# Kernel tuning notes

Hardware: AMD Instinct MI355X
Metric: run time of the kernel (lower is better)

Reference implementation:

```python
import jax, jax.numpy as jnp
import numpy as np
from jax import lax

B, C, H, W = 32, 64, 112, 112
ALPHA, BETA1, BETA2 = 0.25, 1.0, 1.0

# STE sign for weights (DifferntiableSign): fwd = +/-1, bwd mask |w|<=1 (w in [-1,1))
@jax.custom_vjp
def dsign(w):
    return jnp.where(w >= 0, 1.0, -1.0).astype(w.dtype)
def _dsign_fwd(w):
    return dsign(w), w
def _dsign_bwd(w, g):
    return (g * ((w < 1) & (w >= -1)).astype(g.dtype),)
dsign.defvjp(_dsign_fwd, _dsign_bwd)

# ReActNet BinaryActivation: fwd = sign(x), bwd piecewise-polynomial STE
@jax.custom_vjp
def bin_act(x):
    return jnp.where(x >= 0, 1.0, -1.0).astype(x.dtype)
def _ba_fwd(x):
    return bin_act(x), x
def _ba_bwd(x, g):
    slope = jnp.where((x >= -1) & (x < 0), 2.0 + 2.0 * x,
             jnp.where((x >= 0) & (x < 1), 2.0 - 2.0 * x, 0.0))
    return (g * slope.astype(g.dtype),)
bin_act.defvjp(_ba_fwd, _ba_bwd)

def scaled_sign_conv(x, w):
    # per-output-channel scale = mean(|w|) over (in, kh, kw)
    scale = jnp.mean(jnp.abs(w), axis=(1, 2, 3), keepdims=True)
    wb = scale * dsign(w)
    return lax.conv_general_dilated(x, wb, window_strides=(1, 1),
                                    padding=((1, 1), (1, 1)),
                                    dimension_numbers=("NCHW", "OIHW", "NCHW"))

def add_bias(x, b):
    return x + b[None, :, None, None]

def prelu(x, a):
    return jnp.where(x >= 0, x, a[None, :, None, None] * x)

def setup_inputs() -> dict:
    key = jax.random.key(0)
    ks = jax.random.split(key, 12)
    x = jax.random.normal(ks[0], (B, C, H, W), dtype=jnp.float32)
    # conv weights: symmetric uniform in [-1e-3, 1e-3] so signs are nontrivial
    w3 = (jax.random.uniform(ks[1], (C, C, 3, 3)) - 0.5) * 0.002
    w_pw = (jax.random.uniform(ks[2], (C, C, 3, 3)) - 0.5) * 0.002
    b11 = jax.random.normal(ks[3], (C,)) * 0.01
    b12 = jax.random.normal(ks[4], (C,)) * 0.01
    b13 = jax.random.normal(ks[5], (C,)) * 0.01
    b21 = jax.random.normal(ks[6], (C,)) * 0.01
    b22 = jax.random.normal(ks[7], (C,)) * 0.01
    b23 = jax.random.normal(ks[8], (C,)) * 0.01
    a1 = jax.random.uniform(ks[9], (C,), minval=0.1, maxval=0.4)
    a2 = jax.random.uniform(ks[10], (C,), minval=0.1, maxval=0.4)
    return {"x": x, "w3": w3, "w_pw": w_pw, "b11": b11, "b12": b12, "b13": b13,
            "b21": b21, "b22": b22, "b23": b23, "a1": a1, "a2": a2}

def reference(x, w3, w_pw, b11, b12, b13, b21, b22, b23, a1, a2):
    x_in = x * BETA1
    out1 = add_bias(x_in, b11)            # move11
    out1 = bin_act(out1)
    out1 = scaled_sign_conv(out1, w3)     # binary_3x3
    out1 = x + out1 * ALPHA               # stride==1: residual is original x
    out1 = add_bias(out1, b12)            # move12
    out1 = prelu(out1, a1)
    out1 = add_bias(out1, b13)            # move13
    out1_in = out1 * BETA2
    out2 = add_bias(out1_in, b21)         # move21
    out2 = bin_act(out2)
    out2 = scaled_sign_conv(out2, w_pw)   # binary_pw (3x3 per given defaults)
    out2 = out2 * ALPHA + out1
    out2 = add_bias(out2, b22)            # move22
    out2 = prelu(out2, a2)
    out2 = add_bias(out2, b23)            # move23
    return out2
```

## Files before the change

### kernel.cpp

```cpp
#include <hip/hip_runtime.h>
#include <hip/hip_fp16.h>
#include <stdint.h>

#define Bn 32
#define Cc 64
#define Hh 112
#define Ww 112
#define HWp (Hh*Ww)
#define NPIX (Bn*HWp)
#define PW 114
#define PHW (PW*PW)
#define ALPHA 0.25f

#define WB1_OFF   0
#define WB2_OFF   4608
#define ASC1_OFF  9216
#define ASC2_OFF  9472
#define CI1_OFF   9728
#define CI2_OFF   12032
#define BITS1_OFF 16384
#define BITS2_OFF (16384 + 3326976)
#define OUT1H_OFF (16384 + 2*3326976)
#define WS_NEED   (OUT1H_OFF + (size_t)NPIX*Cc*2)

__global__ __launch_bounds__(64) void prep_weights(
        const float* __restrict__ w3, const float* __restrict__ wpw,
        uint64_t* __restrict__ wb1, uint64_t* __restrict__ wb2,
        float* __restrict__ asc1, float* __restrict__ asc2,
        int* __restrict__ ci1, int* __restrict__ ci2) {
    int b = blockIdx.x;
    int lane = threadIdx.x;
    const float* w  = (b < 64) ? w3   : wpw;
    uint64_t* wbits = (b < 64) ? wb1  : wb2;
    float*    ascp  = (b < 64) ? asc1 : asc2;
    int*      cip   = (b < 64) ? ci1  : ci2;
    int o = b & 63;
    const float* wp = w + ((size_t)o * Cc + lane) * 9;
    float v[9]; float asum = 0.f;
    #pragma unroll
    for (int t = 0; t < 9; ++t) { v[t] = wp[t]; asum += fabsf(v[t]); }
    uint64_t bal[9];
    #pragma unroll
    for (int t = 0; t < 9; ++t) bal[t] = __ballot(v[t] < 0.f);
    if (lane < 9) {
        wbits[o * 9 + lane] = bal[lane];
        int ty = lane, tr = ty / 3, tc = ty % 3;
        int sum = 0;
        #pragma unroll
        for (int t = 0; t < 9; ++t) {
            int r = t / 3, c = t % 3;
            bool inv = (tr == 0 && r == 0) || (tr == 2 && r == 2) ||
                       (tc == 0 && c == 0) || (tc == 2 && c == 2);
            if (inv) sum += 64 - 2 * (int)__popcll(bal[t]);
        }
        cip[o * 9 + ty] = 576 - sum;
    }
    #pragma unroll
    for (int off = 32; off > 0; off >>= 1) asum += __shfl_down(asum, off, 64);
    if (lane == 0) ascp[o] = ALPHA * asum * (1.f / 576.f);
}

__global__ __launch_bounds__(256) void pack1(const float* __restrict__ x,
                                             const float* __restrict__ b11,
                                             uint64_t* __restrict__ bits1,
                                             uint64_t* __restrict__ bits2) {
    int pc = blockIdx.x * 256 + threadIdx.x;
    if (pc >= PHW) return;
    int n = blockIdx.y;
    int ph = pc / PW, pw = pc - ph * PW;
    size_t bi = (size_t)n * PHW + pc;
    if (ph == 0 || ph == PW - 1 || pw == 0 || pw == PW - 1) {
        bits1[bi] = 0; bits2[bi] = 0;
        return;
    }
    int hw = (ph - 1) * Ww + (pw - 1);
    const float* xp = x + (size_t)n * Cc * HWp + hw;
    uint64_t m = 0;
    #pragma unroll 1
    for (int cc = 0; cc < Cc; cc += 16) {
        float v[16];
        #pragma unroll
        for (int j = 0; j < 16; ++j) v[j] = xp[(size_t)(cc + j) * HWp];
        #pragma unroll
        for (int j = 0; j < 16; ++j)
            if (v[j] + b11[cc + j] < 0.f) m |= (1ull << (cc + j));
    }
    bits1[bi] = m;
}

template <typename OutT>
__global__ __launch_bounds__(256, 4) void conv1_ep(
        const float* __restrict__ x, const uint64_t* __restrict__ bits1,
        const uint64_t* __restrict__ wb, const float* __restrict__ asc,
        const int* __restrict__ cint,
        const float* __restrict__ b12, const float* __restrict__ a1,
        const float* __restrict__ b13, const float* __restrict__ b21,
        OutT* __restrict__ out1, uint64_t* __restrict__ bits2) {
    __shared__ int lci[Cc * 12];
    for (int i = threadIdx.x; i < Cc * 9; i += 256) {
        int o = i / 9, ty = i - o * 9;
        lci[o * 12 + ty] = cint[i];
    }
    __syncthreads();

    int hw = blockIdx.x * 256 + threadIdx.x;
    int n = blockIdx.y;
    int h = hw / Ww, w = hw - h * Ww;
    int t9 = ((h == 0) ? 0 : (h == Hh - 1) ? 6 : 3) +
             ((w == 0) ? 0 : (w == Ww - 1) ? 2 : 1);

    const uint64_t* bp = bits1 + (size_t)n * PHW + (h + 1) * PW + (w + 1);
    uint64_t w00 = bp[-PW - 1], w01 = bp[-PW], w02 = bp[-PW + 1];
    uint64_t w10 = bp[-1],      w11 = bp[0],   w12 = bp[1];
    uint64_t w20 = bp[PW - 1],  w21 = bp[PW],  w22 = bp[PW + 1];

    const float* xp = x + (size_t)n * Cc * HWp + hw;
    OutT* op = out1 + (size_t)n * Cc * HWp + hw;
    uint64_t m2 = 0;

    float xv[8], xn[8];
    #pragma unroll
    for (int j = 0; j < 8; ++j) xv[j] = xp[(size_t)j * HWp];

    #pragma unroll 1
    for (int oc = 0; oc < Cc; oc += 8) {
        #pragma unroll
        for (int j = 0; j < 8; ++j) xn[j] = xp[(size_t)((oc + 8 + j) & 63) * HWp];
        #pragma unroll
        for (int j = 0; j < 8; ++j) {
            int o = oc + j;
            const uint64_t* wo = wb + o * 9;
            int s;
            s  = (int)__popcll(w00 ^ wo[0]);
            s += (int)__popcll(w01 ^ wo[1]);
            s += (int)__popcll(w02 ^ wo[2]);
            s += (int)__popcll(w10 ^ wo[3]);
            s += (int)__popcll(w11 ^ wo[4]);
            s += (int)__popcll(w12 ^ wo[5]);
            s += (int)__popcll(w20 ^ wo[6]);
            s += (int)__popcll(w21 ^ wo[7]);
            s += (int)__popcll(w22 ^ wo[8]);
            int m = lci[o * 12 + t9] - (s << 1);
            float v = fmaf(asc[o], (float)m, xv[j]);
            v += b12[o];
            v = v >= 0.f ? v : a1[o] * v;
            v += b13[o];
            op[(size_t)o * HWp] = (OutT)v;
            if (v + b21[o] < 0.f) m2 |= (1ull << o);
        }
        #pragma unroll
        for (int j = 0; j < 8; ++j) xv[j] = xn[j];
    }
    bits2[(size_t)n * PHW + (h + 1) * PW + (w + 1)] = m2;
}

template <typename InT>
__global__ __launch_bounds__(256, 4) void conv2_ep(
        const uint64_t* __restrict__ bits2, const InT* __restrict__ out1,
        const uint64_t* __restrict__ wb, const float* __restrict__ asc,
        const int* __restrict__ cint,
        const float* __restrict__ b22, const float* __restrict__ a2,
        const float* __restrict__ b23, float* __restrict__ out) {
    __shared__ int lci[Cc * 12];
    for (int i = threadIdx.x; i < Cc * 9; i += 256) {
        int o = i / 9, ty = i - o * 9;
        lci[o * 12 + ty] = cint[i];
    }
    __syncthreads();

    int hw = blockIdx.x * 256 + threadIdx.x;
    int n = blockIdx.y;
    int h = hw / Ww, w = hw - h * Ww;
    int t9 = ((h == 0) ? 0 : (h == Hh - 1) ? 6 : 3) +
             ((w == 0) ? 0 : (w == Ww - 1) ? 2 : 1);

    const uint64_t* bp = bits2 + (size_t)n * PHW + (h + 1) * PW + (w + 1);
    uint64_t w00 = bp[-PW - 1], w01 = bp[-PW], w02 = bp[-PW + 1];
    uint64_t w10 = bp[-1],      w11 = bp[0],   w12 = bp[1];
    uint64_t w20 = bp[PW - 1],  w21 = bp[PW],  w22 = bp[PW + 1];

    const InT* ip = out1 + (size_t)n * Cc * HWp + hw;
    float* op = out + (size_t)n * Cc * HWp + hw;

    InT rv[8], rn[8];
    #pragma unroll
    for (int j = 0; j < 8; ++j) rv[j] = ip[(size_t)j * HWp];

    #pragma unroll 1
    for (int oc = 0; oc < Cc; oc += 8) {
        #pragma unroll
        for (int j = 0; j < 8; ++j) rn[j] = ip[(size_t)((oc + 8 + j) & 63) * HWp];
        #pragma unroll
        for (int j = 0; j < 8; ++j) {
            int o = oc + j;
            const uint64_t* wo = wb + o * 9;
            int s;
            s  = (int)__popcll(w00 ^ wo[0]);
            s += (int)__popcll(w01 ^ wo[1]);
            s += (int)__popcll(w02 ^ wo[2]);
            s += (int)__popcll(w10 ^ wo[3]);
            s += (int)__popcll(w11 ^ wo[4]);
            s += (int)__popcll(w12 ^ wo[5]);
            s += (int)__popcll(w20 ^ wo[6]);
            s += (int)__popcll(w21 ^ wo[7]);
            s += (int)__popcll(w22 ^ wo[8]);
            int m = lci[o * 12 + t9] - (s << 1);
            float v = fmaf(asc[o], (float)m, (float)rv[j]);
            v += b22[o];
            v = v >= 0.f ? v : a2[o] * v;
            v += b23[o];
            op[(size_t)o * HWp] = v;
        }
        #pragma unroll
        for (int j = 0; j < 8; ++j) rv[j] = rn[j];
    }
}

extern "C" void kernel_launch(void* const* d_in, const int* in_sizes, int n_in,
                              void* d_out, int out_size, void* d_ws, size_t ws_size,
                              hipStream_t stream) {
    const float* x    = (const float*)d_in[0];
    const float* w3   = (const float*)d_in[1];
    const float* wpw  = (const float*)d_in[2];
    const float* b11  = (const float*)d_in[3];
    const float* b12  = (const float*)d_in[4];
    const float* b13  = (const float*)d_in[5];
    const float* b21  = (const float*)d_in[6];
    const float* b22  = (const float*)d_in[7];
    const float* b23  = (const float*)d_in[8];
    const float* a1   = (const float*)d_in[9];
    const float* a2   = (const float*)d_in[10];

    char* ws = (char*)d_ws;
    uint64_t* wb1   = (uint64_t*)(ws + WB1_OFF);
    uint64_t* wb2   = (uint64_t*)(ws + WB2_OFF);
    float*    asc1  = (float*)(ws + ASC1_OFF);
    float*    asc2  = (float*)(ws + ASC2_OFF);
    int*      ci1   = (int*)(ws + CI1_OFF);
    int*      ci2   = (int*)(ws + CI2_OFF);
    uint64_t* bits1 = (uint64_t*)(ws + BITS1_OFF);
    uint64_t* bits2 = (uint64_t*)(ws + BITS2_OFF);
    float*    out   = (float*)d_out;

    dim3 pgrid((PHW + 255) / 256, Bn);
    dim3 cgrid(HWp / 256, Bn);

    prep_weights<<<128, 64, 0, stream>>>(w3, wpw, wb1, wb2, asc1, asc2, ci1, ci2);
    pack1<<<pgrid, 256, 0, stream>>>(x, b11, bits1, bits2);

    if (ws_size >= WS_NEED) {
        __half* out1h = (__half*)(ws + OUT1H_OFF);
        conv1_ep<__half><<<cgrid, 256, 0, stream>>>(x, bits1, wb1, asc1, ci1,
                                                    b12, a1, b13, b21, out1h, bits2);
        conv2_ep<__half><<<cgrid, 256, 0, stream>>>(bits2, out1h, wb2, asc2, ci2,
                                                    b22, a2, b23, out);
    } else {
        conv1_ep<float><<<cgrid, 256, 0, stream>>>(x, bits1, wb1, asc1, ci1,
                                                   b12, a1, b13, b21, out, bits2);
        conv2_ep<float><<<cgrid, 256, 0, stream>>>(bits2, out, wb2, asc2, ci2,
                                                   b22, a2, b23, out);
    }
}
```

Measured before the change: 293.3 us.

## Preload all 64 channel inputs up front and fully unroll the conv loops

In pack1 and both conv kernels, the code now loads all 64 per-channel inputs into registers at once, pinned with empty asm so the compiler cannot sink the loads. It replaces the 8-wide software-pipelined loop with a fully unrolled 64-channel loop. The shared-memory correction table is transposed so each thread reads a contiguous row chosen by its border type. The aim is more memory-level parallelism from issuing all loads before compute, at the cost of higher register pressure that may reduce occupancy or cause spills under launch_bounds(256,4).

```diff
diff --git a/kernel.cpp b/kernel.cpp
--- a/kernel.cpp
+++ b/kernel.cpp
@@ -22,6 +22,8 @@
 #define BITS2_OFF (16384 + 3326976)
 #define OUT1H_OFF (16384 + 2*3326976)
 #define WS_NEED   (OUT1H_OFF + (size_t)NPIX*Cc*2)
+
+#define PIN(v) asm volatile("" : "+v"(v))
 
 __global__ __launch_bounds__(64) void prep_weights(
         const float* __restrict__ w3, const float* __restrict__ wpw,
@@ -60,10 +62,10 @@
     if (lane == 0) ascp[o] = ALPHA * asum * (1.f / 576.f);
 }
 
-__global__ __launch_bounds__(256) void pack1(const float* __restrict__ x,
-                                             const float* __restrict__ b11,
-                                             uint64_t* __restrict__ bits1,
-                                             uint64_t* __restrict__ bits2) {
+__global__ __launch_bounds__(256, 4) void pack1(const float* __restrict__ x,
+                                                const float* __restrict__ b11,
+                                                uint64_t* __restrict__ bits1,
+                                                uint64_t* __restrict__ bits2) {
     int pc = blockIdx.x * 256 + threadIdx.x;
     if (pc >= PHW) return;
     int n = blockIdx.y;
@@ -75,16 +77,15 @@
     }
     int hw = (ph - 1) * Ww + (pw - 1);
     const float* xp = x + (size_t)n * Cc * HWp + hw;
+    float v[Cc];
+    #pragma unroll
+    for (int j = 0; j < Cc; ++j) v[j] = xp[(size_t)j * HWp];
+    #pragma unroll
+    for (int j = 0; j < Cc; ++j) PIN(v[j]);
     uint64_t m = 0;
-    #pragma unroll 1
-    for (int cc = 0; cc < Cc; cc += 16) {
-        float v[16];
-        #pragma unroll
-        for (int j = 0; j < 16; ++j) v[j] = xp[(size_t)(cc + j) * HWp];
-        #pragma unroll
-        for (int j = 0; j < 16; ++j)
-            if (v[j] + b11[cc + j] < 0.f) m |= (1ull << (cc + j));
-    }
+    #pragma unroll
+    for (int j = 0; j < Cc; ++j)
+        if (v[j] + b11[j] < 0.f) m |= (1ull << j);
     bits1[bi] = m;
 }
 
@@ -96,10 +97,10 @@
         const float* __restrict__ b12, const float* __restrict__ a1,
         const float* __restrict__ b13, const float* __restrict__ b21,
         OutT* __restrict__ out1, uint64_t* __restrict__ bits2) {
-    __shared__ int lci[Cc * 12];
+    __shared__ int lci[10 * Cc];
     for (int i = threadIdx.x; i < Cc * 9; i += 256) {
         int o = i / 9, ty = i - o * 9;
-        lci[o * 12 + ty] = cint[i];
+        lci[ty * Cc + o] = cint[i];
     }
     __syncthreads();
 
@@ -108,6 +109,7 @@
     int h = hw / Ww, w = hw - h * Ww;
     int t9 = ((h == 0) ? 0 : (h == Hh - 1) ? 6 : 3) +
              ((w == 0) ? 0 : (w == Ww - 1) ? 2 : 1);
+    const int* lcit = lci + t9 * Cc;
 
     const uint64_t* bp = bits1 + (size_t)n * PHW + (h + 1) * PW + (w + 1);
     uint64_t w00 = bp[-PW - 1], w01 = bp[-PW], w02 = bp[-PW + 1];
@@ -116,40 +118,34 @@
 
     const float* xp = x + (size_t)n * Cc * HWp + hw;
     OutT* op = out1 + (size_t)n * Cc * HWp + hw;
+
+    float xv[Cc];
+    #pragma unroll
+    for (int j = 0; j < Cc; ++j) xv[j] = xp[(size_t)j * HWp];
+    #pragma unroll
+    for (int j = 0; j < Cc; ++j) PIN(xv[j]);
+
     uint64_t m2 = 0;
-
-    float xv[8], xn[8];
-    #pragma unroll
-    for (int j = 0; j < 8; ++j) xv[j] = xp[(size_t)j * HWp];
-
-    #pragma unroll 1
-    for (int oc = 0; oc < Cc; oc += 8) {
-        #pragma unroll
-        for (int j = 0; j < 8; ++j) xn[j] = xp[(size_t)((oc + 8 + j) & 63) * HWp];
-        #pragma unroll
-        for (int j = 0; j < 8; ++j) {
-            int o = oc + j;
-            const uint64_t* wo = wb + o * 9;
-            int s;
-            s  = (int)__popcll(w00 ^ wo[0]);
-            s += (int)__popcll(w01 ^ wo[1]);
-            s += (int)__popcll(w02 ^ wo[2]);
-            s += (int)__popcll(w10 ^ wo[3]);
-            s += (int)__popcll(w11 ^ wo[4]);
-            s += (int)__popcll(w12 ^ wo[5]);
-            s += (int)__popcll(w20 ^ wo[6]);
-            s += (int)__popcll(w21 ^ wo[7]);
-            s += (int)__popcll(w22 ^ wo[8]);
-            int m = lci[o * 12 + t9] - (s << 1);
-            float v = fmaf(asc[o], (float)m, xv[j]);
-            v += b12[o];
-            v = v >= 0.f ? v : a1[o] * v;
-            v += b13[o];
-            op[(size_t)o * HWp] = (OutT)v;
-            if (v + b21[o] < 0.f) m2 |= (1ull << o);
-        }
-        #pragma unroll
-        for (int j = 0; j < 8; ++j) xv[j] = xn[j];
+    #pragma unroll
+    for (int o = 0; o < Cc; ++o) {
+        const uint64_t* wo = wb + o * 9;
+        int s;
+        s  = (int)__popcll(w00 ^ wo[0]);
+        s += (int)__popcll(w01 ^ wo[1]);
+        s += (int)__popcll(w02 ^ wo[2]);
+        s += (int)__popcll(w10 ^ wo[3]);
+        s += (int)__popcll(w11 ^ wo[4]);
+        s += (int)__popcll(w12 ^ wo[5]);
+        s += (int)__popcll(w20 ^ wo[6]);
+        s += (int)__popcll(w21 ^ wo[7]);
+        s += (int)__popcll(w22 ^ wo[8]);
+        int m = lcit[o] - (s << 1);
+        float v = fmaf(asc[o], (float)m, xv[o]);
+        v += b12[o];
+        v = v >= 0.f ? v : a1[o] * v;
+        v += b13[o];
+        op[(size_t)o * HWp] = (OutT)v;
+        if (v + b21[o] < 0.f) m2 |= (1ull << o);
     }
     bits2[(size_t)n * PHW + (h + 1) * PW + (w + 1)] = m2;
 }
@@ -161,10 +157,10 @@
         const int* __restrict__ cint,
         const float* __restrict__ b22, const float* __restrict__ a2,
         const float* __restrict__ b23, float* __restrict__ out) {
-    __shared__ int lci[Cc * 12];
+    __shared__ int lci[10 * Cc];
     for (int i = threadIdx.x; i < Cc * 9; i += 256) {
         int o = i / 9, ty = i - o * 9;
-        lci[o * 12 + ty] = cint[i];
+        lci[ty * Cc + o] = cint[i];
     }
     __syncthreads();
 
@@ -173,6 +169,7 @@
     int h = hw / Ww, w = hw - h * Ww;
     int t9 = ((h == 0) ? 0 : (h == Hh - 1) ? 6 : 3) +
              ((w == 0) ? 0 : (w == Ww - 1) ? 2 : 1);
+    const int* lcit = lci + t9 * Cc;
 
     const uint64_t* bp = bits2 + (size_t)n * PHW + (h + 1) * PW + (w + 1);
     uint64_t w00 = bp[-PW - 1], w01 = bp[-PW], w02 = bp[-PW + 1];
@@ -182,37 +179,31 @@
     const InT* ip = out1 + (size_t)n * Cc * HWp + hw;
     float* op = out + (size_t)n * Cc * HWp + hw;
 
-    InT rv[8], rn[8];
-    #pragma unroll
-    for (int j = 0; j < 8; ++j) rv[j] = ip[(size_t)j * HWp];
-
-    #pragma unroll 1
-    for (int oc = 0; oc < Cc; oc += 8) {
-        #pragma unroll
-        for (int j = 0; j < 8; ++j) rn[j] = ip[(size_t)((oc + 8 + j) & 63) * HWp];
-        #pragma unroll
-        for (int j = 0; j < 8; ++j) {
-            int o = oc + j;
-            const uint64_t* wo = wb + o * 9;
-            int s;
-            s  = (int)__popcll(w00 ^ wo[0]);
-            s += (int)__popcll(w01 ^ wo[1]);
-            s += (int)__popcll(w02 ^ wo[2]);
-            s += (int)__popcll(w10 ^ wo[3]);
-            s += (int)__popcll(w11 ^ wo[4]);
-            s += (int)__popcll(w12 ^ wo[5]);
-            s += (int)__popcll(w20 ^ wo[6]);
-            s += (int)__popcll(w21 ^ wo[7]);
-            s += (int)__popcll(w22 ^ wo[8]);
-            int m = lci[o * 12 + t9] - (s << 1);
-            float v = fmaf(asc[o], (float)m, (float)rv[j]);
-            v += b22[o];
-            v = v >= 0.f ? v : a2[o] * v;
-            v += b23[o];
-            op[(size_t)o * HWp] = v;
-        }
-        #pragma unroll
-        for (int j = 0; j < 8; ++j) rv[j] = rn[j];
+    float rv[Cc];
+    #pragma unroll
+    for (int j = 0; j < Cc; ++j) rv[j] = (float)ip[(size_t)j * HWp];
+    #pragma unroll
+    for (int j = 0; j < Cc; ++j) PIN(rv[j]);
+
+    #pragma unroll
+    for (int o = 0; o < Cc; ++o) {
+        const uint64_t* wo = wb + o * 9;
+        int s;
+        s  = (int)__popcll(w00 ^ wo[0]);
+        s += (int)__popcll(w01 ^ wo[1]);
+        s += (int)__popcll(w02 ^ wo[2]);
+        s += (int)__popcll(w10 ^ wo[3]);
+        s += (int)__popcll(w11 ^ wo[4]);
+        s += (int)__popcll(w12 ^ wo[5]);
+        s += (int)__popcll(w20 ^ wo[6]);
+        s += (int)__popcll(w21 ^ wo[7]);
+        s += (int)__popcll(w22 ^ wo[8]);
+        int m = lcit[o] - (s << 1);
+        float v = fmaf(asc[o], (float)m, rv[o]);
+        v += b22[o];
+        v = v >= 0.f ? v : a2[o] * v;
+        v += b23[o];
+        op[(size_t)o * HWp] = v;
     }
 }
 
```

Result: slower. 312.7 us (+6.6%).

## Process two horizontal pixels per thread with vectorized loads and shared weight reuse

Applied to the files above, without the earlier changes.

Each thread in pack1, conv1 and conv2 now handles two adjacent pixels, using float2/half2 vector loads and stores. The 3x3 bit-neighbourhood becomes a 3x4 window, so bit loads overlap between the two outputs and each weight word is loaded once for both pixels. pack1 now zeroes only the border cells in separate blocks. The final output is written with nontemporal stores, and the correction-count table is repacked to stride 10 with a moved offset. In exchange, per-thread register pressure rises and the grid has half as many threads, which may reduce occupancy.

```diff
diff --git a/kernel.cpp b/kernel.cpp
--- a/kernel.cpp
+++ b/kernel.cpp
@@ -10,18 +10,25 @@
 #define NPIX (Bn*HWp)
 #define PW 114
 #define PHW (PW*PW)
+#define NPAIR (HWp/2)
+#define WROW (Ww/2)
 #define ALPHA 0.25f
+
+typedef float    f32x2 __attribute__((ext_vector_type(2)));
+typedef _Float16 f16x2 __attribute__((ext_vector_type(2)));
 
 #define WB1_OFF   0
 #define WB2_OFF   4608
 #define ASC1_OFF  9216
 #define ASC2_OFF  9472
 #define CI1_OFF   9728
-#define CI2_OFF   12032
+#define CI2_OFF   12288
 #define BITS1_OFF 16384
 #define BITS2_OFF (16384 + 3326976)
 #define OUT1H_OFF (16384 + 2*3326976)
 #define WS_NEED   (OUT1H_OFF + (size_t)NPIX*Cc*2)
+
+#define MEMFENCE() asm volatile("" ::: "memory")
 
 __global__ __launch_bounds__(64) void prep_weights(
         const float* __restrict__ w3, const float* __restrict__ wpw,
@@ -53,39 +60,66 @@
                        (tc == 0 && c == 0) || (tc == 2 && c == 2);
             if (inv) sum += 64 - 2 * (int)__popcll(bal[t]);
         }
-        cip[o * 9 + ty] = 576 - sum;
+        cip[o * 10 + ty] = 576 - sum;
     }
     #pragma unroll
     for (int off = 32; off > 0; off >>= 1) asum += __shfl_down(asum, off, 64);
     if (lane == 0) ascp[o] = ALPHA * asum * (1.f / 576.f);
 }
 
-__global__ __launch_bounds__(256) void pack1(const float* __restrict__ x,
-                                             const float* __restrict__ b11,
-                                             uint64_t* __restrict__ bits1,
-                                             uint64_t* __restrict__ bits2) {
-    int pc = blockIdx.x * 256 + threadIdx.x;
-    if (pc >= PHW) return;
+__global__ __launch_bounds__(256, 4) void pack1(const float* __restrict__ x,
+                                                const float* __restrict__ b11,
+                                                uint64_t* __restrict__ bits1,
+                                                uint64_t* __restrict__ bits2) {
     int n = blockIdx.y;
-    int ph = pc / PW, pw = pc - ph * PW;
-    size_t bi = (size_t)n * PHW + pc;
-    if (ph == 0 || ph == PW - 1 || pw == 0 || pw == PW - 1) {
-        bits1[bi] = 0; bits2[bi] = 0;
+    if (blockIdx.x >= 25) {
+        int t = (blockIdx.x - 25) * 256 + threadIdx.x;
+        if (t < 2 * PW + 2 * Hh) {
+            int cell;
+            if      (t < PW)          cell = t;
+            else if (t < 2 * PW)      cell = 113 * PW + (t - PW);
+            else if (t < 2 * PW + Hh) cell = (t - 2 * PW + 1) * PW;
+            else                      cell = (t - 2 * PW - Hh + 1) * PW + 113;
+            size_t bi = (size_t)n * PHW + cell;
+            bits1[bi] = 0; bits2[bi] = 0;
+        }
         return;
     }
-    int hw = (ph - 1) * Ww + (pw - 1);
+    int p = blockIdx.x * 256 + threadIdx.x;
+    if (p >= NPAIR) return;
+    int h = p / WROW, w0 = (p - h * WROW) * 2;
+    int hw = h * Ww + w0;
     const float* xp = x + (size_t)n * Cc * HWp + hw;
-    uint64_t m = 0;
+    size_t bi = (size_t)n * PHW + (h + 1) * PW + (w0 + 1);
+
+    f32x2 cur[16], nxt[16];
+    #pragma unroll
+    for (int j = 0; j < 16; ++j) cur[j] = *(const f32x2*)(xp + (size_t)j * HWp);
+
+    uint64_t ma = 0, mb = 0;
     #pragma unroll 1
-    for (int cc = 0; cc < Cc; cc += 16) {
-        float v[16];
-        #pragma unroll
-        for (int j = 0; j < 16; ++j) v[j] = xp[(size_t)(cc + j) * HWp];
+    for (int cc = 0; cc < Cc - 16; cc += 16) {
         #pragma unroll
         for (int j = 0; j < 16; ++j)
-            if (v[j] + b11[cc + j] < 0.f) m |= (1ull << (cc + j));
-    }
-    bits1[bi] = m;
+            nxt[j] = *(const f32x2*)(xp + (size_t)(cc + 16 + j) * HWp);
+        MEMFENCE();
+        #pragma unroll
+        for (int j = 0; j < 16; ++j) {
+            float bb = b11[cc + j];
+            if (cur[j].x + bb < 0.f) ma |= (1ull << (cc + j));
+            if (cur[j].y + bb < 0.f) mb |= (1ull << (cc + j));
+        }
+        MEMFENCE();
+        #pragma unroll
+        for (int j = 0; j < 16; ++j) cur[j] = nxt[j];
+    }
+    #pragma unroll
+    for (int j = 0; j < 16; ++j) {
+        float bb = b11[48 + j];
+        if (cur[j].x + bb < 0.f) ma |= (1ull << (48 + j));
+        if (cur[j].y + bb < 0.f) mb |= (1ull << (48 + j));
+    }
+    bits1[bi] = ma; bits1[bi + 1] = mb;
 }
 
 template <typename OutT>
@@ -96,62 +130,77 @@
         const float* __restrict__ b12, const float* __restrict__ a1,
         const float* __restrict__ b13, const float* __restrict__ b21,
         OutT* __restrict__ out1, uint64_t* __restrict__ bits2) {
-    __shared__ int lci[Cc * 12];
-    for (int i = threadIdx.x; i < Cc * 9; i += 256) {
-        int o = i / 9, ty = i - o * 9;
-        lci[o * 12 + ty] = cint[i];
-    }
+    __shared__ int lci[Cc * 10];
+    for (int i = threadIdx.x; i < Cc * 10; i += 256) lci[i] = cint[i];
     __syncthreads();
 
-    int hw = blockIdx.x * 256 + threadIdx.x;
+    int p = blockIdx.x * 256 + threadIdx.x;
+    if (p >= NPAIR) return;
     int n = blockIdx.y;
-    int h = hw / Ww, w = hw - h * Ww;
-    int t9 = ((h == 0) ? 0 : (h == Hh - 1) ? 6 : 3) +
-             ((w == 0) ? 0 : (w == Ww - 1) ? 2 : 1);
-
-    const uint64_t* bp = bits1 + (size_t)n * PHW + (h + 1) * PW + (w + 1);
-    uint64_t w00 = bp[-PW - 1], w01 = bp[-PW], w02 = bp[-PW + 1];
-    uint64_t w10 = bp[-1],      w11 = bp[0],   w12 = bp[1];
-    uint64_t w20 = bp[PW - 1],  w21 = bp[PW],  w22 = bp[PW + 1];
+    int h = p / WROW, w0 = (p - h * WROW) * 2;
+    int hw = h * Ww + w0;
+    int rowp = (h == 0) ? 0 : (h == Hh - 1) ? 6 : 3;
+    int t9a = rowp + ((w0 == 0) ? 0 : 1);
+    int t9b = rowp + ((w0 + 1 == Ww - 1) ? 2 : 1);
+
+    const uint64_t* bp = bits1 + (size_t)n * PHW + (h + 1) * PW + (w0 + 1);
+    uint64_t q0[4], q1[4], q2[4];
+    #pragma unroll
+    for (int c = 0; c < 4; ++c) {
+        q0[c] = bp[-PW - 1 + c]; q1[c] = bp[-1 + c]; q2[c] = bp[PW - 1 + c];
+    }
 
     const float* xp = x + (size_t)n * Cc * HWp + hw;
     OutT* op = out1 + (size_t)n * Cc * HWp + hw;
-    uint64_t m2 = 0;
-
-    float xv[8], xn[8];
-    #pragma unroll
-    for (int j = 0; j < 8; ++j) xv[j] = xp[(size_t)j * HWp];
+    uint64_t m2a = 0, m2b = 0;
+
+    f32x2 cur[8], nxt[8];
+    #pragma unroll
+    for (int j = 0; j < 8; ++j) cur[j] = *(const f32x2*)(xp + (size_t)j * HWp);
 
     #pragma unroll 1
-    for (int oc = 0; oc < Cc; oc += 8) {
-        #pragma unroll
-        for (int j = 0; j < 8; ++j) xn[j] = xp[(size_t)((oc + 8 + j) & 63) * HWp];
+    for (int oc = 0; oc <= Cc - 8; oc += 8) {
+        if (oc < Cc - 8) {
+            #pragma unroll
+            for (int j = 0; j < 8; ++j)
+                nxt[j] = *(const f32x2*)(xp + (size_t)(oc + 8 + j) * HWp);
+        }
+        MEMFENCE();
         #pragma unroll
         for (int j = 0; j < 8; ++j) {
             int o = oc + j;
             const uint64_t* wo = wb + o * 9;
-            int s;
-            s  = (int)__popcll(w00 ^ wo[0]);
-            s += (int)__popcll(w01 ^ wo[1]);
-            s += (int)__popcll(w02 ^ wo[2]);
-            s += (int)__popcll(w10 ^ wo[3]);
-            s += (int)__popcll(w11 ^ wo[4]);
-            s += (int)__popcll(w12 ^ wo[5]);
-            s += (int)__popcll(w20 ^ wo[6]);
-            s += (int)__popcll(w21 ^ wo[7]);
-            s += (int)__popcll(w22 ^ wo[8]);
-            int m = lci[o * 12 + t9] - (s << 1);
-            float v = fmaf(asc[o], (float)m, xv[j]);
-            v += b12[o];
-            v = v >= 0.f ? v : a1[o] * v;
-            v += b13[o];
-            op[(size_t)o * HWp] = (OutT)v;
-            if (v + b21[o] < 0.f) m2 |= (1ull << o);
-        }
-        #pragma unroll
-        for (int j = 0; j < 8; ++j) xv[j] = xn[j];
-    }
-    bits2[(size_t)n * PHW + (h + 1) * PW + (w + 1)] = m2;
+            uint64_t t0 = wo[0], t1 = wo[1], t2 = wo[2], t3 = wo[3], t4 = wo[4],
+                     t5 = wo[5], t6 = wo[6], t7 = wo[7], t8 = wo[8];
+            int sa = (int)__popcll(q0[0] ^ t0) + (int)__popcll(q0[1] ^ t1) + (int)__popcll(q0[2] ^ t2)
+                   + (int)__popcll(q1[0] ^ t3) + (int)__popcll(q1[1] ^ t4) + (int)__popcll(q1[2] ^ t5)
+                   + (int)__popcll(q2[0] ^ t6) + (int)__popcll(q2[1] ^ t7) + (int)__popcll(q2[2] ^ t8);
+            int sb = (int)__popcll(q0[1] ^ t0) + (int)__popcll(q0[2] ^ t1) + (int)__popcll(q0[3] ^ t2)
+                   + (int)__popcll(q1[1] ^ t3) + (int)__popcll(q1[2] ^ t4) + (int)__popcll(q1[3] ^ t5)
+                   + (int)__popcll(q2[1] ^ t6) + (int)__popcll(q2[2] ^ t7) + (int)__popcll(q2[3] ^ t8);
+            int ca = lci[o * 10 + t9a];
+            int cb = lci[o * 10 + t9b];
+            float sc = asc[o], B2 = b12[o], A = a1[o], B3 = b13[o], B1 = b21[o];
+            float va = fmaf(sc, (float)(ca - 2 * sa), cur[j].x);
+            float vb = fmaf(sc, (float)(cb - 2 * sb), cur[j].y);
+            va += B2; va = va >= 0.f ? va : A * va; va += B3;
+            vb += B2; vb = vb >= 0.f ? vb : A * vb; vb += B3;
+            if constexpr (sizeof(OutT) == 2) {
+                f16x2 hv; hv.x = (_Float16)va; hv.y = (_Float16)vb;
+                *(f16x2*)(op + (size_t)o * HWp) = hv;
+            } else {
+                f32x2 fv; fv.x = va; fv.y = vb;
+                *(f32x2*)(op + (size_t)o * HWp) = fv;
+            }
+            if (va + B1 < 0.f) m2a |= (1ull << o);
+            if (vb + B1 < 0.f) m2b |= (1ull << o);
+        }
+        MEMFENCE();
+        #pragma unroll
+        for (int j = 0; j < 8; ++j) cur[j] = nxt[j];
+    }
+    size_t b2 = (size_t)n * PHW + (h + 1) * PW + (w0 + 1);
+    bits2[b2] = m2a; bits2[b2 + 1] = m2b;
 }
 
 template <typename InT>
@@ -161,58 +210,86 @@
         const int* __restrict__ cint,
         const float* __restrict__ b22, const float* __restrict__ a2,
         const float* __restrict__ b23, float* __restrict__ out) {
-    __shared__ int lci[Cc * 12];
-    for (int i = threadIdx.x; i < Cc * 9; i += 256) {
-        int o = i / 9, ty = i - o * 9;
-        lci[o * 12 + ty] = cint[i];
-    }
+    __shared__ int lci[Cc * 10];
+    for (int i = threadIdx.x; i < Cc * 10; i += 256) lci[i] = cint[i];
     __syncthreads();
 
-    int hw = blockIdx.x * 256 + threadIdx.x;
+    int p = blockIdx.x * 256 + threadIdx.x;
+    if (p >= NPAIR) return;
     int n = blockIdx.y;
-    int h = hw / Ww, w = hw - h * Ww;
-    int t9 = ((h == 0) ? 0 : (h == Hh - 1) ? 6 : 3) +
-             ((w == 0) ? 0 : (w == Ww - 1) ? 2 : 1);
-
-    const uint64_t* bp = bits2 + (size_t)n * PHW + (h + 1) * PW + (w + 1);
-    uint64_t w00 = bp[-PW - 1], w01 = bp[-PW], w02 = bp[-PW + 1];
-    uint64_t w10 = bp[-1],      w11 = bp[0],   w12 = bp[1];
-    uint64_t w20 = bp[PW - 1],  w21 = bp[PW],  w22 = bp[PW + 1];
+    int h = p / WROW, w0 = (p - h * WROW) * 2;
+    int hw = h * Ww + w0;
+    int rowp = (h == 0) ? 0 : (h == Hh - 1) ? 6 : 3;
+    int t9a = rowp + ((w0 == 0) ? 0 : 1);
+    int t9b = rowp + ((w0 + 1 == Ww - 1) ? 2 : 1);
+
+    const uint64_t* bp = bits2 + (size_t)n * PHW + (h + 1) * PW + (w0 + 1);
+    uint64_t q0[4], q1[4], q2[4];
+    #pragma unroll
+    for (int c = 0; c < 4; ++c) {
+        q0[c] = bp[-PW - 1 + c]; q1[c] = bp[-1 + c]; q2[c] = bp[PW - 1 + c];
+    }
 
     const InT* ip = out1 + (size_t)n * Cc * HWp + hw;
     float* op = out + (size_t)n * Cc * HWp + hw;
 
-    InT rv[8], rn[8];
-    #pragma unroll
-    for (int j = 0; j < 8; ++j) rv[j] = ip[(size_t)j * HWp];
+    f16x2 curh[8], nxth[8];
+    f32x2 curf[8], nxtf[8];
+    if constexpr (sizeof(InT) == 2) {
+        #pragma unroll
+        for (int j = 0; j < 8; ++j) curh[j] = *(const f16x2*)(ip + (size_t)j * HWp);
+    } else {
+        #pragma unroll
+        for (int j = 0; j < 8; ++j) curf[j] = *(const f32x2*)(ip + (size_t)j * HWp);
+    }
 
     #pragma unroll 1
-    for (int oc = 0; oc < Cc; oc += 8) {
-        #pragma unroll
-        for (int j = 0; j < 8; ++j) rn[j] = ip[(size_t)((oc + 8 + j) & 63) * HWp];
+    for (int oc = 0; oc <= Cc - 8; oc += 8) {
+        if (oc < Cc - 8) {
+            if constexpr (sizeof(InT) == 2) {
+                #pragma unroll
+                for (int j = 0; j < 8; ++j)
+                    nxth[j] = *(const f16x2*)(ip + (size_t)(oc + 8 + j) * HWp);
+            } else {
+                #pragma unroll
+                for (int j = 0; j < 8; ++j)
+                    nxtf[j] = *(const f32x2*)(ip + (size_t)(oc + 8 + j) * HWp);
+            }
+        }
+        MEMFENCE();
         #pragma unroll
         for (int j = 0; j < 8; ++j) {
             int o = oc + j;
             const uint64_t* wo = wb + o * 9;
-            int s;
-            s  = (int)__popcll(w00 ^ wo[0]);
-            s += (int)__popcll(w01 ^ wo[1]);
-            s += (int)__popcll(w02 ^ wo[2]);
-            s += (int)__popcll(w10 ^ wo[3]);
-            s += (int)__popcll(w11 ^ wo[4]);
-            s += (int)__popcll(w12 ^ wo[5]);
-            s += (int)__popcll(w20 ^ wo[6]);
-            s += (int)__popcll(w21 ^ wo[7]);
-            s += (int)__popcll(w22 ^ wo[8]);
-            int m = lci[o * 12 + t9] - (s << 1);
-            float v = fmaf(asc[o], (float)m, (float)rv[j]);
-            v += b22[o];
-            v = v >= 0.f ? v : a2[o] * v;
-            v += b23[o];
-            op[(size_t)o * HWp] = v;
-        }
-        #pragma unroll
-        for (int j = 0; j < 8; ++j) rv[j] = rn[j];
+            uint64_t t0 = wo[0], t1 = wo[1], t2 = wo[2], t3 = wo[3], t4 = wo[4],
+                     t5 = wo[5], t6 = wo[6], t7 = wo[7], t8 = wo[8];
+            int sa = (int)__popcll(q0[0] ^ t0) + (int)__popcll(q0[1] ^ t1) + (int)__popcll(q0[2] ^ t2)
+                   + (int)__popcll(q1[0] ^ t3) + (int)__popcll(q1[1] ^ t4) + (int)__popcll(q1[2] ^ t5)
+                   + (int)__popcll(q2[0] ^ t6) + (int)__popcll(q2[1] ^ t7) + (int)__popcll(q2[2] ^ t8);
+            int sb = (int)__popcll(q0[1] ^ t0) + (int)__popcll(q0[2] ^ t1) + (int)__popcll(q0[3] ^ t2)
+                   + (int)__popcll(q1[1] ^ t3) + (int)__popcll(q1[2] ^ t4) + (int)__popcll(q1[3] ^ t5)
+                   + (int)__popcll(q2[1] ^ t6) + (int)__popcll(q2[2] ^ t7) + (int)__popcll(q2[3] ^ t8);
+            int ca = lci[o * 10 + t9a];
+            int cb = lci[o * 10 + t9b];
+            float ra, rb;
+            if constexpr (sizeof(InT) == 2) { ra = (float)curh[j].x; rb = (float)curh[j].y; }
+            else                            { ra = curf[j].x;        rb = curf[j].y; }
+            float sc = asc[o], B2 = b22[o], A = a2[o], B3 = b23[o];
+            float va = fmaf(sc, (float)(ca - 2 * sa), ra);
+            float vb = fmaf(sc, (float)(cb - 2 * sb), rb);
+            va += B2; va = va >= 0.f ? va : A * va; va += B3;
+            vb += B2; vb = vb >= 0.f ? vb : A * vb; vb += B3;
+            f32x2 fv; fv.x = va; fv.y = vb;
+            __builtin_nontemporal_store(fv, (f32x2*)(op + (size_t)o * HWp));
+        }
+        MEMFENCE();
+        if constexpr (sizeof(InT) == 2) {
+            #pragma unroll
+            for (int j = 0; j < 8; ++j) curh[j] = nxth[j];
+        } else {
+            #pragma unroll
+            for (int j = 0; j < 8; ++j) curf[j] = nxtf[j];
+        }
     }
 }
 
@@ -242,8 +319,8 @@
     uint64_t* bits2 = (uint64_t*)(ws + BITS2_OFF);
     float*    out   = (float*)d_out;
 
-    dim3 pgrid((PHW + 255) / 256, Bn);
-    dim3 cgrid(HWp / 256, Bn);
+    dim3 pgrid(27, Bn);
+    dim3 cgrid((NPAIR + 255) / 256, Bn);
 
     prep_weights<<<128, 64, 0, stream>>>(w3, wpw, wb1, wb2, asc1, asc2, ci1, ci2);
     pack1<<<pgrid, 256, 0, stream>>>(x, b11, bits1, bits2);
```

New measurement: 294.7 us. No clear change (+0.5%).

## Fuse sign packing and both binary convs into one spatially tiled kernel

Applied to the files above, without the earlier changes.

Replaces the pack, conv1 and conv2 kernels with a single kernel per 16x16 tile. It packs sign bits for a 20x20 halo region into LDS, computes the first conv plus epilogue and re-packs a 18x18 halo of bits, keeping the intermediate residual as fp16 in registers. This removes the global round trips for the bit planes and the fp16 intermediate and cuts two launches. In exchange the halo ring costs redundant conv1 work in a few threads, which may diverge, and register pressure rises from holding 32 packed fp16 residuals.

```diff
diff --git a/kernel.cpp b/kernel.cpp
--- a/kernel.cpp
+++ b/kernel.cpp
@@ -7,21 +7,30 @@
 #define Hh 112
 #define Ww 112
 #define HWp (Hh*Ww)
-#define NPIX (Bn*HWp)
-#define PW 114
-#define PHW (PW*PW)
 #define ALPHA 0.25f
+
+#define TS 16
+#define NT 7
+#define RA 20
+#define RB 18
+
+typedef _Float16 f16x2 __attribute__((ext_vector_type(2)));
 
 #define WB1_OFF   0
 #define WB2_OFF   4608
 #define ASC1_OFF  9216
 #define ASC2_OFF  9472
 #define CI1_OFF   9728
-#define CI2_OFF   12032
-#define BITS1_OFF 16384
-#define BITS2_OFF (16384 + 3326976)
-#define OUT1H_OFF (16384 + 2*3326976)
-#define WS_NEED   (OUT1H_OFF + (size_t)NPIX*Cc*2)
+#define CI2_OFF   12288
+
+#define MEMFENCE() asm volatile("" ::: "memory")
+
+__device__ __forceinline__ int dot9(const uint64_t* q, const uint64_t* __restrict__ wo) {
+    int s = 0;
+    #pragma unroll
+    for (int k = 0; k < 9; ++k) s += (int)__popcll(q[k] ^ wo[k]);
+    return s;
+}
 
 __global__ __launch_bounds__(64) void prep_weights(
         const float* __restrict__ w3, const float* __restrict__ wpw,
@@ -53,166 +62,172 @@
                        (tc == 0 && c == 0) || (tc == 2 && c == 2);
             if (inv) sum += 64 - 2 * (int)__popcll(bal[t]);
         }
-        cip[o * 9 + ty] = 576 - sum;
+        cip[o * 10 + ty] = 576 - sum;
     }
     #pragma unroll
     for (int off = 32; off > 0; off >>= 1) asum += __shfl_down(asum, off, 64);
     if (lane == 0) ascp[o] = ALPHA * asum * (1.f / 576.f);
 }
 
-__global__ __launch_bounds__(256) void pack1(const float* __restrict__ x,
-                                             const float* __restrict__ b11,
-                                             uint64_t* __restrict__ bits1,
-                                             uint64_t* __restrict__ bits2) {
-    int pc = blockIdx.x * 256 + threadIdx.x;
-    if (pc >= PHW) return;
-    int n = blockIdx.y;
-    int ph = pc / PW, pw = pc - ph * PW;
-    size_t bi = (size_t)n * PHW + pc;
-    if (ph == 0 || ph == PW - 1 || pw == 0 || pw == PW - 1) {
-        bits1[bi] = 0; bits2[bi] = 0;
-        return;
-    }
-    int hw = (ph - 1) * Ww + (pw - 1);
-    const float* xp = x + (size_t)n * Cc * HWp + hw;
-    uint64_t m = 0;
-    #pragma unroll 1
-    for (int cc = 0; cc < Cc; cc += 16) {
-        float v[16];
-        #pragma unroll
-        for (int j = 0; j < 16; ++j) v[j] = xp[(size_t)(cc + j) * HWp];
-        #pragma unroll
-        for (int j = 0; j < 16; ++j)
-            if (v[j] + b11[cc + j] < 0.f) m |= (1ull << (cc + j));
-    }
-    bits1[bi] = m;
-}
-
-template <typename OutT>
-__global__ __launch_bounds__(256, 4) void conv1_ep(
-        const float* __restrict__ x, const uint64_t* __restrict__ bits1,
-        const uint64_t* __restrict__ wb, const float* __restrict__ asc,
-        const int* __restrict__ cint,
+__global__ __launch_bounds__(256, 4) void fused(
+        const float* __restrict__ x,
+        const uint64_t* __restrict__ wb1, const uint64_t* __restrict__ wb2,
+        const float* __restrict__ asc1, const float* __restrict__ asc2,
+        const int* __restrict__ ci1, const int* __restrict__ ci2,
+        const float* __restrict__ b11,
         const float* __restrict__ b12, const float* __restrict__ a1,
         const float* __restrict__ b13, const float* __restrict__ b21,
-        OutT* __restrict__ out1, uint64_t* __restrict__ bits2) {
-    __shared__ int lci[Cc * 12];
-    for (int i = threadIdx.x; i < Cc * 9; i += 256) {
-        int o = i / 9, ty = i - o * 9;
-        lci[o * 12 + ty] = cint[i];
+        const float* __restrict__ b22, const float* __restrict__ a2,
+        const float* __restrict__ b23,
+        float* __restrict__ out) {
+    __shared__ uint64_t lb1[RA * RA];
+    __shared__ uint64_t lb2[RB * RB];
+    __shared__ int lc1[Cc * 10];
+    __shared__ int lc2[Cc * 10];
+
+    int tid = threadIdx.x;
+    int bx = blockIdx.x;
+    int n  = blockIdx.y;
+    int tyy = bx / NT, txx = bx - tyy * NT;
+    int h0 = tyy * TS, w0 = txx * TS;
+
+    for (int i = tid; i < Cc * 10; i += 256) { lc1[i] = ci1[i]; lc2[i] = ci2[i]; }
+
+    const float* xn = x + (size_t)n * Cc * HWp;
+
+    #pragma unroll
+    for (int it = 0; it < 2; ++it) {
+        int idx = tid + it * 256;
+        if (idx < RA * RA) {
+            int ai = idx / RA, aj = idx - ai * RA;
+            int ph = h0 - 2 + ai, pw = w0 - 2 + aj;
+            uint64_t m = 0;
+            if ((unsigned)ph < (unsigned)Hh && (unsigned)pw < (unsigned)Ww) {
+                const float* xp = xn + ph * Ww + pw;
+                float v[32];
+                #pragma unroll
+                for (int j = 0; j < 32; ++j) v[j] = xp[(size_t)j * HWp];
+                MEMFENCE();
+                #pragma unroll
+                for (int j = 0; j < 32; ++j)
+                    if (v[j] + b11[j] < 0.f) m |= (1ull << j);
+                #pragma unroll
+                for (int j = 0; j < 32; ++j) v[j] = xp[(size_t)(32 + j) * HWp];
+                MEMFENCE();
+                #pragma unroll
+                for (int j = 0; j < 32; ++j)
+                    if (v[j] + b11[32 + j] < 0.f) m |= (1ull << (32 + j));
+            }
+            lb1[idx] = m;
+        }
     }
     __syncthreads();
 
-    int hw = blockIdx.x * 256 + threadIdx.x;
-    int n = blockIdx.y;
-    int h = hw / Ww, w = hw - h * Ww;
-    int t9 = ((h == 0) ? 0 : (h == Hh - 1) ? 6 : 3) +
-             ((w == 0) ? 0 : (w == Ww - 1) ? 2 : 1);
-
-    const uint64_t* bp = bits1 + (size_t)n * PHW + (h + 1) * PW + (w + 1);
-    uint64_t w00 = bp[-PW - 1], w01 = bp[-PW], w02 = bp[-PW + 1];
-    uint64_t w10 = bp[-1],      w11 = bp[0],   w12 = bp[1];
-    uint64_t w20 = bp[PW - 1],  w21 = bp[PW],  w22 = bp[PW + 1];
-
-    const float* xp = x + (size_t)n * Cc * HWp + hw;
-    OutT* op = out1 + (size_t)n * Cc * HWp + hw;
-    uint64_t m2 = 0;
-
-    float xv[8], xn[8];
-    #pragma unroll
-    for (int j = 0; j < 8; ++j) xv[j] = xp[(size_t)j * HWp];
-
-    #pragma unroll 1
-    for (int oc = 0; oc < Cc; oc += 8) {
-        #pragma unroll
-        for (int j = 0; j < 8; ++j) xn[j] = xp[(size_t)((oc + 8 + j) & 63) * HWp];
-        #pragma unroll
-        for (int j = 0; j < 8; ++j) {
-            int o = oc + j;
-            const uint64_t* wo = wb + o * 9;
-            int s;
-            s  = (int)__popcll(w00 ^ wo[0]);
-            s += (int)__popcll(w01 ^ wo[1]);
-            s += (int)__popcll(w02 ^ wo[2]);
-            s += (int)__popcll(w10 ^ wo[3]);
-            s += (int)__popcll(w11 ^ wo[4]);
-            s += (int)__popcll(w12 ^ wo[5]);
-            s += (int)__popcll(w20 ^ wo[6]);
-            s += (int)__popcll(w21 ^ wo[7]);
-            s += (int)__popcll(w22 ^ wo[8]);
-            int m = lci[o * 12 + t9] - (s << 1);
-            float v = fmaf(asc[o], (float)m, xv[j]);
-            v += b12[o];
-            v = v >= 0.f ? v : a1[o] * v;
-            v += b13[o];
-            op[(size_t)o * HWp] = (OutT)v;
-            if (v + b21[o] < 0.f) m2 |= (1ull << o);
-        }
-        #pragma unroll
-        for (int j = 0; j < 8; ++j) xv[j] = xn[j];
-    }
-    bits2[(size_t)n * PHW + (h + 1) * PW + (w + 1)] = m2;
-}
-
-template <typename InT>
-__global__ __launch_bounds__(256, 4) void conv2_ep(
-        const uint64_t* __restrict__ bits2, const InT* __restrict__ out1,
-        const uint64_t* __restrict__ wb, const float* __restrict__ asc,
-        const int* __restrict__ cint,
-        const float* __restrict__ b22, const float* __restrict__ a2,
-        const float* __restrict__ b23, float* __restrict__ out) {
-    __shared__ int lci[Cc * 12];
-    for (int i = threadIdx.x; i < Cc * 9; i += 256) {
-        int o = i / 9, ty = i - o * 9;
-        lci[o * 12 + ty] = cint[i];
+    int py = tid >> 4, px = tid & 15;
+    int ph = h0 + py, pw = w0 + px;
+    int t9i = ((ph == 0) ? 0 : (ph == Hh - 1) ? 6 : 3) +
+              ((pw == 0) ? 0 : (pw == Ww - 1) ? 2 : 1);
+
+    f16x2 res[32];
+    {
+        int bi = py + 1, bj = px + 1;
+        uint64_t q[9];
+        #pragma unroll
+        for (int r = 0; r < 3; ++r)
+            #pragma unroll
+            for (int c = 0; c < 3; ++c)
+                q[r * 3 + c] = lb1[(bi + r) * RA + (bj + c)];
+
+        const float* xp = xn + ph * Ww + pw;
+        uint64_t m2 = 0;
+        #pragma unroll
+        for (int oc = 0; oc < Cc; oc += 8) {
+            float xv[8];
+            #pragma unroll
+            for (int j = 0; j < 8; ++j) xv[j] = xp[(size_t)(oc + j) * HWp];
+            MEMFENCE();
+            #pragma unroll
+            for (int j = 0; j < 8; ++j) {
+                int ch = oc + j;
+                int s = dot9(q, wb1 + ch * 9);
+                int m = lc1[ch * 10 + t9i] - (s << 1);
+                float v = fmaf(asc1[ch], (float)m, xv[j]);
+                v += b12[ch];
+                v = fmaf(fminf(v, 0.f), a1[ch] - 1.0f, v);
+                v += b13[ch];
+                if (j & 1) res[ch >> 1].y = (_Float16)v;
+                else       res[ch >> 1].x = (_Float16)v;
+                if (v + b21[ch] < 0.f) m2 |= (1ull << ch);
+            }
+        }
+        lb2[bi * RB + bj] = m2;
+    }
+
+    if (tid < 2 * RB + 2 * (RB - 2)) {
+        int ri, rj;
+        if      (tid < RB)          { ri = 0;            rj = tid; }
+        else if (tid < 2 * RB)      { ri = RB - 1;       rj = tid - RB; }
+        else if (tid < 2 * RB + 16) { ri = tid - 2 * RB + 1;      rj = 0; }
+        else                        { ri = tid - (2 * RB + 16) + 1; rj = RB - 1; }
+        int rph = h0 - 1 + ri, rpw = w0 - 1 + rj;
+        uint64_t m2 = 0;
+        if ((unsigned)rph < (unsigned)Hh && (unsigned)rpw < (unsigned)Ww) {
+            int t9r = ((rph == 0) ? 0 : (rph == Hh - 1) ? 6 : 3) +
+                      ((rpw == 0) ? 0 : (rpw == Ww - 1) ? 2 : 1);
+            uint64_t q[9];
+            #pragma unroll
+            for (int r = 0; r < 3; ++r)
+                #pragma unroll
+                for (int c = 0; c < 3; ++c)
+                    q[r * 3 + c] = lb1[(ri + r) * RA + (rj + c)];
+            const float* xp = xn + rph * Ww + rpw;
+            #pragma unroll 1
+            for (int oc = 0; oc < Cc; oc += 8) {
+                float xv[8];
+                #pragma unroll
+                for (int j = 0; j < 8; ++j) xv[j] = xp[(size_t)(oc + j) * HWp];
+                MEMFENCE();
+                #pragma unroll
+                for (int j = 0; j < 8; ++j) {
+                    int ch = oc + j;
+                    int s = dot9(q, wb1 + ch * 9);
+                    int m = lc1[ch * 10 + t9r] - (s << 1);
+                    float v = fmaf(asc1[ch], (float)m, xv[j]);
+                    v += b12[ch];
+                    v = fmaf(fminf(v, 0.f), a1[ch] - 1.0f, v);
+                    v += b13[ch];
+                    if (v + b21[ch] < 0.f) m2 |= (1ull << ch);
+                }
+            }
+        }
+        lb2[ri * RB + rj] = m2;
     }
     __syncthreads();
 
-    int hw = blockIdx.x * 256 + threadIdx.x;
-    int n = blockIdx.y;
-    int h = hw / Ww, w = hw - h * Ww;
-    int t9 = ((h == 0) ? 0 : (h == Hh - 1) ? 6 : 3) +
-             ((w == 0) ? 0 : (w == Ww - 1) ? 2 : 1);
-
-    const uint64_t* bp = bits2 + (size_t)n * PHW + (h + 1) * PW + (w + 1);
-    uint64_t w00 = bp[-PW - 1], w01 = bp[-PW], w02 = bp[-PW + 1];
-    uint64_t w10 = bp[-1],      w11 = bp[0],   w12 = bp[1];
-    uint64_t w20 = bp[PW - 1],  w21 = bp[PW],  w22 = bp[PW + 1];
-
-    const InT* ip = out1 + (size_t)n * Cc * HWp + hw;
-    float* op = out + (size_t)n * Cc * HWp + hw;
-
-    InT rv[8], rn[8];
-    #pragma unroll
-    for (int j = 0; j < 8; ++j) rv[j] = ip[(size_t)j * HWp];
-
-    #pragma unroll 1
-    for (int oc = 0; oc < Cc; oc += 8) {
-        #pragma unroll
-        for (int j = 0; j < 8; ++j) rn[j] = ip[(size_t)((oc + 8 + j) & 63) * HWp];
-        #pragma unroll
-        for (int j = 0; j < 8; ++j) {
-            int o = oc + j;
-            const uint64_t* wo = wb + o * 9;
-            int s;
-            s  = (int)__popcll(w00 ^ wo[0]);
-            s += (int)__popcll(w01 ^ wo[1]);
-            s += (int)__popcll(w02 ^ wo[2]);
-            s += (int)__popcll(w10 ^ wo[3]);
-            s += (int)__popcll(w11 ^ wo[4]);
-            s += (int)__popcll(w12 ^ wo[5]);
-            s += (int)__popcll(w20 ^ wo[6]);
-            s += (int)__popcll(w21 ^ wo[7]);
-            s += (int)__popcll(w22 ^ wo[8]);
-            int m = lci[o * 12 + t9] - (s << 1);
-            float v = fmaf(asc[o], (float)m, (float)rv[j]);
-            v += b22[o];
-            v = v >= 0.f ? v : a2[o] * v;
-            v += b23[o];
-            op[(size_t)o * HWp] = v;
-        }
-        #pragma unroll
-        for (int j = 0; j < 8; ++j) rv[j] = rn[j];
+    {
+        uint64_t q[9];
+        #pragma unroll
+        for (int r = 0; r < 3; ++r)
+            #pragma unroll
+            for (int c = 0; c < 3; ++c)
+                q[r * 3 + c] = lb2[(py + r) * RB + (px + c)];
+
+        float* op = out + (size_t)n * Cc * HWp + ph * Ww + pw;
+        #pragma unroll
+        for (int oc = 0; oc < Cc; oc += 8) {
+            #pragma unroll
+            for (int j = 0; j < 8; ++j) {
+                int ch = oc + j;
+                int s = dot9(q, wb2 + ch * 9);
+                int m = lc2[ch * 10 + t9i] - (s << 1);
+                float r = (j & 1) ? (float)res[ch >> 1].y : (float)res[ch >> 1].x;
+                float v = fmaf(asc2[ch], (float)m, r);
+                v += b22[ch];
+                v = fmaf(fminf(v, 0.f), a2[ch] - 1.0f, v);
+                v += b23[ch];
+                __builtin_nontemporal_store(v, op + (size_t)ch * HWp);
+            }
+        }
     }
 }
 
@@ -238,26 +253,11 @@
     float*    asc2  = (float*)(ws + ASC2_OFF);
     int*      ci1   = (int*)(ws + CI1_OFF);
     int*      ci2   = (int*)(ws + CI2_OFF);
-    uint64_t* bits1 = (uint64_t*)(ws + BITS1_OFF);
-    uint64_t* bits2 = (uint64_t*)(ws + BITS2_OFF);
     float*    out   = (float*)d_out;
 
-    dim3 pgrid((PHW + 255) / 256, Bn);
-    dim3 cgrid(HWp / 256, Bn);
-
     prep_weights<<<128, 64, 0, stream>>>(w3, wpw, wb1, wb2, asc1, asc2, ci1, ci2);
-    pack1<<<pgrid, 256, 0, stream>>>(x, b11, bits1, bits2);
-
-    if (ws_size >= WS_NEED) {
-        __half* out1h = (__half*)(ws + OUT1H_OFF);
-        conv1_ep<__half><<<cgrid, 256, 0, stream>>>(x, bits1, wb1, asc1, ci1,
-                                                    b12, a1, b13, b21, out1h, bits2);
-        conv2_ep<__half><<<cgrid, 256, 0, stream>>>(bits2, out1h, wb2, asc2, ci2,
-                                                    b22, a2, b23, out);
-    } else {
-        conv1_ep<float><<<cgrid, 256, 0, stream>>>(x, bits1, wb1, asc1, ci1,
-                                                   b12, a1, b13, b21, out, bits2);
-        conv2_ep<float><<<cgrid, 256, 0, stream>>>(bits2, out, wb2, asc2, ci2,
-                                                   b22, a2, b23, out);
-    }
-}
+
+    dim3 fgrid(NT * NT, Bn);
+    fused<<<fgrid, 256, 0, stream>>>(x, wb1, wb2, asc1, asc2, ci1, ci2,
+                                     b11, b12, a1, b13, b21, b22, a2, b23, out);
+}
```

Result: slower. 341.4 us (+16.4%).
